# Performance work log

Measured on AMD Instinct MI355X. Metric: run time of the kernel, lower is better.

## Reference

```python
import jax, jax.numpy as jnp
import numpy as np


def _patches(x, k, pad):
    # x: [B,C,H,W] -> [B,C,k*k,Ho,Wo]
    if pad:
        x = jnp.pad(x, ((0, 0), (0, 0), (pad, pad), (pad, pad)))
    B, C, H, W = x.shape
    Ho, Wo = H - k + 1, W - k + 1
    cols = [x[:, :, i:i + Ho, j:j + Wo] for i in range(k) for j in range(k)]
    return jnp.stack(cols, axis=2)


def _tropical_conv(x, w, pad, reduce_fn):
    # y[b,o,h,w] = sum_c reduce_k ( x_patch[b,c,k,h,w] + w[o,c,k] )
    k = w.shape[-1]
    p = _patches(x, k, pad)                                   # [B,C,KK,Ho,Wo]
    wf = w.reshape(w.shape[0], w.shape[1], k * k)             # [O,C,KK]
    s = p[:, None] + wf[None, :, :, :, None, None]            # [B,O,C,KK,Ho,Wo]
    return reduce_fn(s, axis=3).sum(axis=2)                   # [B,O,Ho,Wo]


def _avgpool2(x):
    B, C, H, W = x.shape
    return x.reshape(B, C, H // 2, 2, W // 2, 2).mean(axis=(3, 5))


def setup_inputs() -> dict:
    key = jax.random.key(0)
    ks = jax.random.split(key, 9)
    return {
        "input": jax.random.normal(ks[0], (256, 1, 28, 28), jnp.float32),
        "w1": jax.random.normal(ks[1], (6, 1, 5, 5), jnp.float32),
        "w2": jax.random.normal(ks[2], (16, 6, 5, 5), jnp.float32),
        "fw1": jax.random.normal(ks[3], (120, 400), jnp.float32) * 0.05,
        "fb1": jax.random.normal(ks[4], (120,), jnp.float32) * 0.05,
        "fw2": jax.random.normal(ks[5], (84, 120), jnp.float32) * 0.05,
        "fb2": jax.random.normal(ks[6], (84,), jnp.float32) * 0.05,
        "fw3": jax.random.normal(ks[7], (10, 84), jnp.float32) * 0.05,
        "fb3": jax.random.normal(ks[8], (10,), jnp.float32) * 0.05,
    }


def reference(input, w1, w2, fw1, fb1, fw2, fb2, fw3, fb3):
    x = _tropical_conv(input, w1, pad=2, reduce_fn=jnp.min)   # [B,6,28,28]
    x = _avgpool2(x)                                          # [B,6,14,14]
    x = _tropical_conv(x, w2, pad=0, reduce_fn=jnp.max)       # [B,16,10,10]
    x = _avgpool2(x)                                          # [B,16,5,5]
    x = x.reshape(x.shape[0], -1)                             # [B,400]
    x = jax.nn.relu(x @ fw1.T + fb1)
    x = jax.nn.relu(x @ fw2.T + fb2)
    return x @ fw3.T + fb3                                    # [B,10]
```

## Files before the change

kernel.cpp:

```cpp
#include <hip/hip_runtime.h>

__global__ __launch_bounds__(256) void lenet_fused(
    const float* __restrict__ input,
    const float* __restrict__ w1,
    const float* __restrict__ w2,
    const float* __restrict__ fw1,
    const float* __restrict__ fb1,
    const float* __restrict__ fw2,
    const float* __restrict__ fb2,
    const float* __restrict__ fw3,
    const float* __restrict__ fb3,
    float* __restrict__ out)
{
    __shared__ float sIn[32 * 32];
    __shared__ float sW1[150];
    __shared__ float sW2[2400];
    __shared__ float sX1[6 * 14 * 14];
    __shared__ float sX2[400];
    __shared__ float sH1[120];
    __shared__ float sH2[84];

    const int tid = threadIdx.x;
    const int b = blockIdx.x;

    for (int i = tid; i < 150; i += 256) sW1[i] = w1[i];
    for (int i = tid; i < 2400; i += 256) sW2[i] = w2[i];

    const float* inb = input + b * 784;
    for (int i = tid; i < 1024; i += 256) {
        int r = (i >> 5) - 2, c = (i & 31) - 2;
        float v = 0.f;
        if ((unsigned)r < 28u && (unsigned)c < 28u) v = inb[r * 28 + c];
        sIn[i] = v;
    }
    __syncthreads();

    for (int idx = tid; idx < 6 * 14 * 14; idx += 256) {
        int o = idx / 196;
        int r = idx % 196;
        int ph = r / 14, pw = r % 14;
        const float* w = sW1 + o * 25;
        float acc = 0.f;
        #pragma unroll
        for (int dy = 0; dy < 2; ++dy) {
            #pragma unroll
            for (int dx = 0; dx < 2; ++dx) {
                int h = 2 * ph + dy, wc = 2 * pw + dx;
                float m = 1e30f;
                #pragma unroll
                for (int i = 0; i < 5; ++i) {
                    #pragma unroll
                    for (int j = 0; j < 5; ++j) {
                        m = fminf(m, sIn[(h + i) * 32 + (wc + j)] + w[i * 5 + j]);
                    }
                }
                acc += m;
            }
        }
        sX1[idx] = acc * 0.25f;
    }
    __syncthreads();

    for (int idx = tid; idx < 400; idx += 256) {
        int o = idx / 25;
        int r = idx % 25;
        int ph = r / 5, pw = r % 5;
        float acc = 0.f;
        #pragma unroll
        for (int dy = 0; dy < 2; ++dy) {
            #pragma unroll
            for (int dx = 0; dx < 2; ++dx) {
                int h = 2 * ph + dy, wc = 2 * pw + dx;
                float s = 0.f;
                for (int c = 0; c < 6; ++c) {
                    const float* x = sX1 + c * 196 + h * 14 + wc;
                    const float* w = sW2 + (o * 6 + c) * 25;
                    float m = -1e30f;
                    #pragma unroll
                    for (int i = 0; i < 5; ++i) {
                        #pragma unroll
                        for (int j = 0; j < 5; ++j) {
                            m = fmaxf(m, x[i * 14 + j] + w[i * 5 + j]);
                        }
                    }
                    s += m;
                }
                acc += s;
            }
        }
        sX2[idx] = acc * 0.25f;
    }
    __syncthreads();

    if (tid < 120) {
        const float* w = fw1 + tid * 400;
        float a0 = 0.f, a1 = 0.f, a2 = 0.f, a3 = 0.f;
        for (int k = 0; k < 400; k += 4) {
            a0 += sX2[k] * w[k];
            a1 += sX2[k + 1] * w[k + 1];
            a2 += sX2[k + 2] * w[k + 2];
            a3 += sX2[k + 3] * w[k + 3];
        }
        sH1[tid] = fmaxf((a0 + a1) + (a2 + a3) + fb1[tid], 0.f);
    }
    __syncthreads();

    if (tid < 84) {
        const float* w = fw2 + tid * 120;
        float acc = fb2[tid];
        for (int k = 0; k < 120; ++k) acc += sH1[k] * w[k];
        sH2[tid] = fmaxf(acc, 0.f);
    }
    __syncthreads();

    if (tid < 10) {
        const float* w = fw3 + tid * 84;
        float acc = fb3[tid];
        for (int k = 0; k < 84; ++k) acc += sH2[k] * w[k];
        out[b * 10 + tid] = acc;
    }
}

extern "C" void kernel_launch(void* const* d_in, const int* in_sizes, int n_in,
                              void* d_out, int out_size, void* d_ws, size_t ws_size,
                              hipStream_t stream) {
    const float* input = (const float*)d_in[0];
    const float* w1  = (const float*)d_in[1];
    const float* w2  = (const float*)d_in[2];
    const float* fw1 = (const float*)d_in[3];
    const float* fb1 = (const float*)d_in[4];
    const float* fw2 = (const float*)d_in[5];
    const float* fb2 = (const float*)d_in[6];
    const float* fw3 = (const float*)d_in[7];
    const float* fb3 = (const float*)d_in[8];
    float* out = (float*)d_out;

    lenet_fused<<<256, 256, 0, stream>>>(input, w1, w2, fw1, fb1, fw2, fb2,
                                         fw3, fb3, out);
}
```

Baseline: 91.43 us.

## Restructure conv stages with register-blocked sliding windows and 1024-thread blocks

Raises the block size to 1024 threads and rewrites both tropical convolutions so each thread keeps the 5x5 filter in registers and slides down a column, producing 7 or 10 outputs per thread. Each input row is read once and reused across several outputs instead of reloading 25 values per output. Pooling is split into separate passes over full-resolution shared buffers, the second conv is parallelised across input channels, and the FC layers use split-K partial sums followed by a reduction. The cost is more barriers, a larger aliased shared-memory buffer, and higher register pressure per thread.

```diff
diff --git a/kernel.cpp b/kernel.cpp
--- a/kernel.cpp
+++ b/kernel.cpp
@@ -1,6 +1,9 @@
 #include <hip/hip_runtime.h>
 
-__global__ __launch_bounds__(256) void lenet_fused(
+
+#define POS_INF 1e30f
+
+__global__ __launch_bounds__(1024, 4) void lenet_fused(
     const float* __restrict__ input,
     const float* __restrict__ w1,
     const float* __restrict__ w2,
@@ -12,112 +15,161 @@
     const float* __restrict__ fb3,
     float* __restrict__ out)
 {
-    __shared__ float sIn[32 * 32];
-    __shared__ float sW1[150];
-    __shared__ float sW2[2400];
-    __shared__ float sX1[6 * 14 * 14];
-    __shared__ float sX2[400];
-    __shared__ float sH1[120];
-    __shared__ float sH2[84];
+    __shared__ float smem[13930];
+    float* sW1 = smem;
+    float* sW2 = smem + 150;
+    float* sX1 = smem + 2550;
+    float* sX2 = smem + 3726;
+    float* sH1 = smem + 4126;
+    float* sH2 = smem + 4246;
+    float* A   = smem + 4330;
+    float* sIn = A;
+    float* sP1 = A + 1024;
+    float* sP2 = A;
+    float* sR1 = A;
+    float* sR2 = A + 960;
+    float* sR3 = A + 1296;
 
     const int tid = threadIdx.x;
     const int b = blockIdx.x;
 
-    for (int i = tid; i < 150; i += 256) sW1[i] = w1[i];
-    for (int i = tid; i < 2400; i += 256) sW2[i] = w2[i];
-
-    const float* inb = input + b * 784;
-    for (int i = tid; i < 1024; i += 256) {
-        int r = (i >> 5) - 2, c = (i & 31) - 2;
+    if (tid < 150) sW1[tid] = w1[tid];
+    for (int i = tid; i < 2400; i += 1024) sW2[i] = w2[i];
+    {
+        int r = (tid >> 5) - 2, c = (tid & 31) - 2;
         float v = 0.f;
-        if ((unsigned)r < 28u && (unsigned)c < 28u) v = inb[r * 28 + c];
-        sIn[i] = v;
+        if ((unsigned)r < 28u && (unsigned)c < 28u) v = input[b * 784 + r * 28 + c];
+        sIn[tid] = v;
     }
     __syncthreads();
 
-    for (int idx = tid; idx < 6 * 14 * 14; idx += 256) {
-        int o = idx / 196;
-        int r = idx % 196;
-        int ph = r / 14, pw = r % 14;
-        const float* w = sW1 + o * 25;
-        float acc = 0.f;
+    if (tid < 672) {
+        int o = tid / 112, rem = tid % 112, g = rem / 28, j0 = rem % 28;
+        float w[25];
         #pragma unroll
-        for (int dy = 0; dy < 2; ++dy) {
+        for (int k = 0; k < 25; ++k) w[k] = sW1[o * 25 + k];
+        float acc[7];
+        #pragma unroll
+        for (int h = 0; h < 7; ++h) acc[h] = POS_INF;
+        const float* xb = sIn + (7 * g) * 32 + j0;
+        #pragma unroll
+        for (int r = 0; r < 11; ++r) {
+            float x0 = xb[r*32+0], x1 = xb[r*32+1], x2 = xb[r*32+2],
+                  x3 = xb[r*32+3], x4 = xb[r*32+4];
             #pragma unroll
-            for (int dx = 0; dx < 2; ++dx) {
-                int h = 2 * ph + dy, wc = 2 * pw + dx;
-                float m = 1e30f;
-                #pragma unroll
-                for (int i = 0; i < 5; ++i) {
-                    #pragma unroll
-                    for (int j = 0; j < 5; ++j) {
-                        m = fminf(m, sIn[(h + i) * 32 + (wc + j)] + w[i * 5 + j]);
-                    }
+            for (int h = 0; h < 7; ++h) {
+                if (h <= r && r <= h + 4) {
+                    const int i = r - h;
+                    acc[h] = fminf(acc[h], x0 + w[i*5+0]);
+                    acc[h] = fminf(acc[h], x1 + w[i*5+1]);
+                    acc[h] = fminf(acc[h], x2 + w[i*5+2]);
+                    acc[h] = fminf(acc[h], x3 + w[i*5+3]);
+                    acc[h] = fminf(acc[h], x4 + w[i*5+4]);
                 }
-                acc += m;
             }
         }
-        sX1[idx] = acc * 0.25f;
+        #pragma unroll
+        for (int h = 0; h < 7; ++h)
+            sP1[(o * 28 + 7 * g + h) * 28 + j0] = acc[h];
     }
     __syncthreads();
 
-    for (int idx = tid; idx < 400; idx += 256) {
-        int o = idx / 25;
-        int r = idx % 25;
-        int ph = r / 5, pw = r % 5;
-        float acc = 0.f;
-        #pragma unroll
-        for (int dy = 0; dy < 2; ++dy) {
-            #pragma unroll
-            for (int dx = 0; dx < 2; ++dx) {
-                int h = 2 * ph + dy, wc = 2 * pw + dx;
-                float s = 0.f;
-                for (int c = 0; c < 6; ++c) {
-                    const float* x = sX1 + c * 196 + h * 14 + wc;
-                    const float* w = sW2 + (o * 6 + c) * 25;
-                    float m = -1e30f;
-                    #pragma unroll
-                    for (int i = 0; i < 5; ++i) {
-                        #pragma unroll
-                        for (int j = 0; j < 5; ++j) {
-                            m = fmaxf(m, x[i * 14 + j] + w[i * 5 + j]);
-                        }
-                    }
-                    s += m;
-                }
-                acc += s;
-            }
-        }
-        sX2[idx] = acc * 0.25f;
+    for (int idx = tid; idx < 1176; idx += 1024) {
+        int o = idx / 196, rem = idx % 196, ph = rem / 14, pw = rem % 14;
+        const float* p = sP1 + (o * 28 + 2 * ph) * 28 + 2 * pw;
+        sX1[idx] = 0.25f * (p[0] + p[1] + p[28] + p[29]);
     }
     __syncthreads();
 
-    if (tid < 120) {
-        const float* w = fw1 + tid * 400;
-        float a0 = 0.f, a1 = 0.f, a2 = 0.f, a3 = 0.f;
-        for (int k = 0; k < 400; k += 4) {
-            a0 += sX2[k] * w[k];
-            a1 += sX2[k + 1] * w[k + 1];
-            a2 += sX2[k + 2] * w[k + 2];
-            a3 += sX2[k + 3] * w[k + 3];
+    if (tid < 960) {
+        int o = tid / 60, rem = tid % 60, c = rem / 10, j0 = rem % 10;
+        float w[25];
+        #pragma unroll
+        for (int k = 0; k < 25; ++k) w[k] = sW2[(o * 6 + c) * 25 + k];
+        float acc[10];
+        #pragma unroll
+        for (int h = 0; h < 10; ++h) acc[h] = -POS_INF;
+        const float* xb = sX1 + c * 196 + j0;
+        #pragma unroll
+        for (int r = 0; r < 14; ++r) {
+            float x0 = xb[r*14+0], x1 = xb[r*14+1], x2 = xb[r*14+2],
+                  x3 = xb[r*14+3], x4 = xb[r*14+4];
+            #pragma unroll
+            for (int h = 0; h < 10; ++h) {
+                if (h <= r && r <= h + 4) {
+                    const int i = r - h;
+                    acc[h] = fmaxf(acc[h], x0 + w[i*5+0]);
+                    acc[h] = fmaxf(acc[h], x1 + w[i*5+1]);
+                    acc[h] = fmaxf(acc[h], x2 + w[i*5+2]);
+                    acc[h] = fmaxf(acc[h], x3 + w[i*5+3]);
+                    acc[h] = fmaxf(acc[h], x4 + w[i*5+4]);
+                }
+            }
         }
-        sH1[tid] = fmaxf((a0 + a1) + (a2 + a3) + fb1[tid], 0.f);
+        float* dst = sP2 + (o * 6 + c) * 100 + j0;
+        #pragma unroll
+        for (int h = 0; h < 10; ++h) dst[h * 10] = acc[h];
     }
     __syncthreads();
 
-    if (tid < 84) {
-        const float* w = fw2 + tid * 120;
-        float acc = fb2[tid];
-        for (int k = 0; k < 120; ++k) acc += sH1[k] * w[k];
-        sH2[tid] = fmaxf(acc, 0.f);
+    if (tid < 400) {
+        int o = tid / 25, rem = tid % 25, ph = rem / 5, pw = rem % 5;
+        float s = 0.f;
+        #pragma unroll
+        for (int c = 0; c < 6; ++c) {
+            const float* p = sP2 + (o * 6 + c) * 100 + (2 * ph) * 10 + 2 * pw;
+            s += p[0] + p[1] + p[10] + p[11];
+        }
+        sX2[tid] = 0.25f * s;
     }
     __syncthreads();
 
+    if (tid < 960) {
+        int n = tid >> 3, s8 = tid & 7;
+        const float* w = fw1 + n * 400 + s8 * 50;
+        const float* x = sX2 + s8 * 50;
+        float a = 0.f;
+        #pragma unroll 10
+        for (int k = 0; k < 50; ++k) a += x[k] * w[k];
+        sR1[tid] = a;
+    }
+    __syncthreads();
+    if (tid < 120) {
+        const float* p = sR1 + tid * 8;
+        float a = p[0]+p[1]+p[2]+p[3]+p[4]+p[5]+p[6]+p[7] + fb1[tid];
+        sH1[tid] = fmaxf(a, 0.f);
+    }
+    __syncthreads();
+
+    if (tid < 336) {
+        int n = tid >> 2, s4 = tid & 3;
+        const float* w = fw2 + n * 120 + s4 * 30;
+        const float* x = sH1 + s4 * 30;
+        float a = 0.f;
+        #pragma unroll 10
+        for (int k = 0; k < 30; ++k) a += x[k] * w[k];
+        sR2[tid] = a;
+    }
+    __syncthreads();
+    if (tid < 84) {
+        const float* p = sR2 + tid * 4;
+        sH2[tid] = fmaxf(p[0] + p[1] + p[2] + p[3] + fb2[tid], 0.f);
+    }
+    __syncthreads();
+
+    if (tid < 40) {
+        int n = tid >> 2, s4 = tid & 3;
+        const float* w = fw3 + n * 84 + s4 * 21;
+        const float* x = sH2 + s4 * 21;
+        float a = 0.f;
+        #pragma unroll 7
+        for (int k = 0; k < 21; ++k) a += x[k] * w[k];
+        sR3[tid] = a;
+    }
+    __syncthreads();
     if (tid < 10) {
-        const float* w = fw3 + tid * 84;
-        float acc = fb3[tid];
-        for (int k = 0; k < 84; ++k) acc += sH2[k] * w[k];
-        out[b * 10 + tid] = acc;
+        const float* p = sR3 + tid * 4;
+        out[b * 10 + tid] = p[0] + p[1] + p[2] + p[3] + fb3[tid];
     }
 }
 
@@ -135,6 +187,6 @@
     const float* fb3 = (const float*)d_in[8];
     float* out = (float*)d_out;
 
-    lenet_fused<<<256, 256, 0, stream>>>(input, w1, w2, fw1, fb1, fw2, fb2,
-                                         fw3, fb3, out);
+    lenet_fused<<<256, 1024, 0, stream>>>(input, w1, w2, fw1, fb1, fw2, fb2,
+                                          fw3, fb3, out);
 }
```

New measurement: 86.80 us. 5.1% less time.
